# Performance work log

Hardware: AMD Instinct MI355X
Metric: run time of the kernel (lower is better)

Reference implementation:

```python
import jax, jax.numpy as jnp
import numpy as np

NUM_EXPERTS = 8
TOPK = 2
INPUT_DIM = 2048
OUTPUT_DIM = 2048


def setup_inputs() -> dict:
    key = jax.random.key(0)
    k_x, k_w, k_gw, k_gb = jax.random.split(key, 4)
    x = jax.random.normal(k_x, (8192, INPUT_DIM), dtype=jnp.float32)
    # experts: Linear(input_dim, output_dim*num_experts), xavier_uniform weight, zero bias
    fan_out = OUTPUT_DIM * NUM_EXPERTS
    limit = float(np.sqrt(6.0 / (INPUT_DIM + fan_out)))
    expert_w = jax.random.uniform(k_w, (fan_out, INPUT_DIM), minval=-limit, maxval=limit, dtype=jnp.float32)
    expert_b = jnp.zeros((fan_out,), dtype=jnp.float32)
    # gate: Linear(input_dim, num_experts), default torch init (uniform +-1/sqrt(fan_in))
    gl = 1.0 / float(np.sqrt(INPUT_DIM))
    gate_w = jax.random.uniform(k_gw, (NUM_EXPERTS, INPUT_DIM), minval=-gl, maxval=gl, dtype=jnp.float32)
    gate_b = jax.random.uniform(k_gb, (NUM_EXPERTS,), minval=-gl, maxval=gl, dtype=jnp.float32)
    return {"x": x, "expert_w": expert_w, "expert_b": expert_b, "gate_w": gate_w, "gate_b": gate_b}


def reference(x, expert_w, expert_b, gate_w, gate_b):
    B = x.shape[0]
    # gating
    gate_logits = x @ gate_w.T + gate_b                      # [B, E]
    gate_probs = jax.nn.softmax(gate_logits, axis=-1)
    top_k_probs, top_k_idx = jax.lax.top_k(gate_probs, TOPK)  # [B, K]
    # dense expert GEMM: all experts computed
    expert_out = x @ expert_w.T + expert_b                   # [B, E*D_out]
    expert_out = expert_out.reshape(B, NUM_EXPERTS, OUTPUT_DIM)
    # gather selected experts per token and combine
    sel = jnp.take_along_axis(expert_out, top_k_idx[:, :, None], axis=1)  # [B, K, D_out]
    out = jnp.sum(sel * top_k_probs[:, :, None], axis=1)     # [B, D_out]
    return out
```

## Files before the change

kernel.cpp:

```cpp
#include <hip/hip_runtime.h>

#define NUM_TOKENS 8192
#define DIM 2048
#define NE 8
#define BM 128
#define BN 128
#define BK 64

typedef __bf16 bf16x8 __attribute__((ext_vector_type(8)));
typedef float f32x4 __attribute__((ext_vector_type(4)));

typedef __attribute__((address_space(1))) const void* as1_cvp;
typedef __attribute__((address_space(3))) void* as3_vp;

__device__ __forceinline__ unsigned short f2bf(float f) {
  unsigned int u = __float_as_uint(f);
  unsigned int lsb = (u >> 16) & 1u;
  u += 0x7fffu + lsb;
  return (unsigned short)(u >> 16);
}
__device__ __forceinline__ float bflo(unsigned int u) {
  return __uint_as_float(u << 16);
}
__device__ __forceinline__ float bfhi(unsigned int u) {
  return __uint_as_float(u & 0xffff0000u);
}

__global__ __launch_bounds__(256) void convert_w_kernel(
    const float4* __restrict__ w, ushort4* __restrict__ wb) {
  int i = blockIdx.x * 256 + threadIdx.x;
  float4 v = w[i];
  ushort4 o;
  o.x = f2bf(v.x); o.y = f2bf(v.y); o.z = f2bf(v.z); o.w = f2bf(v.w);
  wb[i] = o;
}

__global__ __launch_bounds__(256) void gating_kernel(
    const float* __restrict__ x, const float* __restrict__ gw,
    const float* __restrict__ gb, unsigned short* __restrict__ xb,
    float* __restrict__ probs, int* __restrict__ routed) {
  const int wave = threadIdx.x >> 6;
  const int lane = threadIdx.x & 63;
  const int t = blockIdx.x * 4 + wave;
  const float4* xrow = (const float4*)(x + (size_t)t * DIM);
  ushort4* xbrow = (ushort4*)(xb + (size_t)t * DIM);
  float acc[NE];
#pragma unroll
  for (int e = 0; e < NE; ++e) acc[e] = 0.f;
#pragma unroll
  for (int it = 0; it < DIM / (4 * 64); ++it) {
    const int k4 = it * 64 + lane;
    float4 xv = xrow[k4];
    ushort4 o;
    o.x = f2bf(xv.x); o.y = f2bf(xv.y); o.z = f2bf(xv.z); o.w = f2bf(xv.w);
    xbrow[k4] = o;
#pragma unroll
    for (int e = 0; e < NE; ++e) {
      float4 wv = ((const float4*)(gw + (size_t)e * DIM))[k4];
      acc[e] += xv.x * wv.x + xv.y * wv.y + xv.z * wv.z + xv.w * wv.w;
    }
  }
#pragma unroll
  for (int e = 0; e < NE; ++e) {
#pragma unroll
    for (int off = 32; off > 0; off >>= 1)
      acc[e] += __shfl_xor(acc[e], off, 64);
  }
  if (lane == 0) {
    float p[NE];
    float mx = -1e30f;
#pragma unroll
    for (int e = 0; e < NE; ++e) {
      p[e] = acc[e] + gb[e];
      mx = fmaxf(mx, p[e]);
    }
    float s = 0.f;
#pragma unroll
    for (int e = 0; e < NE; ++e) { p[e] = __expf(p[e] - mx); s += p[e]; }
    float inv = 1.f / s;
#pragma unroll
    for (int e = 0; e < NE; ++e) p[e] *= inv;
    int e0 = 0;
#pragma unroll
    for (int e = 1; e < NE; ++e) if (p[e] > p[e0]) e0 = e;
    int e1 = (e0 == 0) ? 1 : 0;
#pragma unroll
    for (int e = 0; e < NE; ++e) if (e != e0 && p[e] > p[e1]) e1 = e;
    probs[t * 2 + 0] = p[e0];
    probs[t * 2 + 1] = p[e1];
    routed[t] = e0 | (e1 << 8);
  }
}

__global__ __launch_bounds__(256) void build_lists_kernel(
    const int* __restrict__ routed, int* __restrict__ lists,
    int* __restrict__ counts, int* __restrict__ tokpos) {
  const int e = blockIdx.x;
  const int tid = threadIdx.x;
  __shared__ int sc[256];
  __shared__ int sb[256];
  const int base_t = tid * (NUM_TOKENS / 256);
  int c = 0, cb = 0;
#pragma unroll 4
  for (int j = 0; j < NUM_TOKENS / 256; ++j) {
    int r = routed[base_t + j];
    int a0 = r & 0xff, a1 = (r >> 8) & 0xff;
    c += (a0 == e) + (a1 == e);
    cb += (a0 < e) + (a1 < e);
  }
  sc[tid] = c;
  sb[tid] = cb;
  __syncthreads();
  for (int ofs = 1; ofs < 256; ofs <<= 1) {
    int v = (tid >= ofs) ? sc[tid - ofs] : 0;
    int w = (tid >= ofs) ? sb[tid - ofs] : 0;
    __syncthreads();
    sc[tid] += v;
    sb[tid] += w;
    __syncthreads();
  }
  const int ebase = sb[255];
  int pos = sc[tid] - c;
#pragma unroll 4
  for (int j = 0; j < NUM_TOKENS / 256; ++j) {
    int t = base_t + j;
    int r = routed[t];
    if ((r & 0xff) == e) {
      lists[e * NUM_TOKENS + pos] = t;
      tokpos[2 * t] = ebase + pos;
      pos++;
    }
    if (((r >> 8) & 0xff) == e) {
      lists[e * NUM_TOKENS + pos] = t | 0x10000;
      tokpos[2 * t + 1] = ebase + pos;
      pos++;
    }
  }
  if (tid == 255) {
    counts[e] = sc[255];
    counts[8 + e] = ebase;
  }
}

__global__ __launch_bounds__(256) void moe_gemm_kernel(
    const unsigned short* __restrict__ xb,
    const unsigned short* __restrict__ wb,
    const float* __restrict__ eb,
    const float* __restrict__ probs,
    const int* __restrict__ lists,
    const int* __restrict__ counts,
    unsigned short* __restrict__ y,
    float* __restrict__ out,
    int use_y) {
  const int e = blockIdx.z;
  const int cnt = counts[e];
  const int s = blockIdx.x + 16 * blockIdx.y;
  const int xcd = s & 7;
  const int j = s >> 3;
  const int R = (j >> 4) * 8 + xcd;
  const int w4 = j & 15;
  const int mt = (R >> 2) * 4 + (w4 & 3);
  const int nt = (R & 3) * 4 + (w4 >> 2);
  const int m0 = mt * BM;
  if (m0 >= cnt) return;
  const int n0 = nt * BN;

  __shared__ __attribute__((aligned(16))) unsigned short As[BM * BK];
  __shared__ __attribute__((aligned(16))) unsigned short Bs[BN * BK];

  const int tid = threadIdx.x;
  const int wave = tid >> 6;
  const int lane = tid & 63;
  const int srow = lane >> 3;
  const int scol = ((lane & 7) ^ srow) * 8;

  const unsigned short* ag[4];
  const unsigned short* bg[4];
#pragma unroll
  for (int i = 0; i < 4; ++i) {
    int r = m0 + wave * 32 + i * 8 + srow;
    int rc = r < cnt ? r : cnt - 1;
    int tok = lists[e * NUM_TOKENS + rc] & 0xFFFF;
    ag[i] = xb + (size_t)tok * DIM + scol;
    int wr = e * DIM + n0 + wave * 32 + i * 8 + srow;
    bg[i] = wb + (size_t)wr * DIM + scol;
  }

  const f32x4 zero = {0.f, 0.f, 0.f, 0.f};
  f32x4 acc[4][4];
#pragma unroll
  for (int a = 0; a < 4; ++a)
#pragma unroll
    for (int b = 0; b < 4; ++b) acc[a][b] = zero;

  const int wm = (wave >> 1) * 64;
  const int wn = (wave & 1) * 64;
  const int frow = lane & 15;
  const int csel = lane >> 4;
  const int swz = lane & 7;

  for (int k0 = 0; k0 < DIM; k0 += BK) {
    __syncthreads();
#pragma unroll
    for (int i = 0; i < 4; ++i) {
      __builtin_amdgcn_global_load_lds(
          (as1_cvp)(ag[i] + k0),
          (as3_vp)(As + (wave * 32 + i * 8) * BK), 16, 0, 0);
      __builtin_amdgcn_global_load_lds(
          (as1_cvp)(bg[i] + k0),
          (as3_vp)(Bs + (wave * 32 + i * 8) * BK), 16, 0, 0);
    }
    __syncthreads();
#pragma unroll
    for (int kk = 0; kk < BK; kk += 32) {
      const int koff = ((((kk >> 3) | csel) ^ swz) << 3);
      bf16x8 af[4], bfr[4];
#pragma unroll
      for (int im = 0; im < 4; ++im)
        af[im] = *(const bf16x8*)(As + (wm + im * 16 + frow) * BK + koff);
#pragma unroll
      for (int in_ = 0; in_ < 4; ++in_)
        bfr[in_] = *(const bf16x8*)(Bs + (wn + in_ * 16 + frow) * BK + koff);
#pragma unroll
      for (int im = 0; im < 4; ++im)
#pragma unroll
        for (int in_ = 0; in_ < 4; ++in_)
          acc[im][in_] = __builtin_amdgcn_mfma_f32_16x16x32_bf16(
              af[im], bfr[in_], acc[im][in_], 0, 0, 0);
    }
  }

  const int quad = lane >> 4;
  const int col = lane & 15;
  const int ybase = counts[8 + e];
#pragma unroll
  for (int im = 0; im < 4; ++im) {
#pragma unroll
    for (int reg = 0; reg < 4; ++reg) {
      int r = m0 + wm + im * 16 + quad * 4 + reg;
      if (r >= cnt) continue;
      if (use_y) {
        unsigned short* yrow = y + (size_t)(ybase + r) * DIM;
#pragma unroll
        for (int in_ = 0; in_ < 4; ++in_) {
          int n = n0 + wn + in_ * 16 + col;
          yrow[n] = f2bf(acc[im][in_][reg] + eb[e * DIM + n]);
        }
      } else {
        int entry = lists[e * NUM_TOKENS + r];
        int tok = entry & 0xFFFF;
        int slot = entry >> 16;
        float p = probs[tok * 2 + slot];
        float* orow = out + (size_t)tok * DIM;
#pragma unroll
        for (int in_ = 0; in_ < 4; ++in_) {
          int n = n0 + wn + in_ * 16 + col;
          float v = acc[im][in_][reg] + eb[e * DIM + n];
          atomicAdd(orow + n, p * v);
        }
      }
    }
  }
}

__global__ __launch_bounds__(256) void combine_kernel(
    const unsigned short* __restrict__ y, const float* __restrict__ probs,
    const int* __restrict__ tokpos, float* __restrict__ out) {
  const int t = blockIdx.x;
  const int tid = threadIdx.x;
  const int i0 = tokpos[2 * t], i1 = tokpos[2 * t + 1];
  const float p0 = probs[2 * t], p1 = probs[2 * t + 1];
  uint4 a = ((const uint4*)(y + (size_t)i0 * DIM))[tid];
  uint4 b = ((const uint4*)(y + (size_t)i1 * DIM))[tid];
  float4 o0, o1;
  o0.x = p0 * bflo(a.x) + p1 * bflo(b.x);
  o0.y = p0 * bfhi(a.x) + p1 * bfhi(b.x);
  o0.z = p0 * bflo(a.y) + p1 * bflo(b.y);
  o0.w = p0 * bfhi(a.y) + p1 * bfhi(b.y);
  o1.x = p0 * bflo(a.z) + p1 * bflo(b.z);
  o1.y = p0 * bfhi(a.z) + p1 * bfhi(b.z);
  o1.z = p0 * bflo(a.w) + p1 * bflo(b.w);
  o1.w = p0 * bfhi(a.w) + p1 * bfhi(b.w);
  float4* orow = (float4*)(out + (size_t)t * DIM);
  orow[2 * tid] = o0;
  orow[2 * tid + 1] = o1;
}

extern "C" void kernel_launch(void* const* d_in, const int* in_sizes, int n_in,
                              void* d_out, int out_size, void* d_ws, size_t ws_size,
                              hipStream_t stream) {
  const float* x  = (const float*)d_in[0];
  const float* ew = (const float*)d_in[1];
  const float* eb = (const float*)d_in[2];
  const float* gw = (const float*)d_in[3];
  const float* gb = (const float*)d_in[4];
  float* out = (float*)d_out;
  char* p = (char*)d_ws;

  const size_t NEED = 67108864ull + 33554432ull + 67108864ull + 65536ull +
                      262144ull + 64ull + 32768ull + 65536ull;
  const int use_y = (ws_size >= NEED) ? 1 : 0;

  unsigned short* wb = (unsigned short*)p; p += 67108864;
  unsigned short* xb = (unsigned short*)p; p += 33554432;
  unsigned short* y = nullptr;
  if (use_y) { y = (unsigned short*)p; p += 67108864; }
  float* probs = (float*)p; p += 65536;
  int* lists   = (int*)p;   p += 262144;
  int* counts  = (int*)p;   p += 64;
  int* routed  = (int*)p;   p += 32768;
  int* tokpos  = (int*)p;   p += 65536;

  if (!use_y)
    hipMemsetAsync(out, 0, (size_t)NUM_TOKENS * DIM * sizeof(float), stream);
  convert_w_kernel<<<(NE * DIM * DIM / 4) / 256, 256, 0, stream>>>(
      (const float4*)ew, (ushort4*)wb);
  gating_kernel<<<NUM_TOKENS / 4, 256, 0, stream>>>(x, gw, gb, xb, probs,
                                                    routed);
  build_lists_kernel<<<NE, 256, 0, stream>>>(routed, lists, counts, tokpos);
  moe_gemm_kernel<<<dim3(DIM / BN, NUM_TOKENS / BM, NE), 256, 0, stream>>>(
      xb, wb, eb, probs, lists, counts, y, out, use_y);
  if (use_y)
    combine_kernel<<<NUM_TOKENS, 256, 0, stream>>>(y, probs, tokpos, out);
}
```

Baseline: 505.5 us.

## Fuse weight conversion into gating kernel, vectorize GEMM epilogue, widen list builder

Merges the weight bf16 conversion and the gating/x-conversion into one launch, removing a kernel boundary and letting the two memory-bound phases overlap. Swaps the MFMA operands so each lane holds four consecutive output columns, which allows 8-byte vectorized bf16 stores and float4 bias loads in the epilogue in place of scattered 2-byte stores. Doubles the build_lists block to 512 threads to shorten each thread's serial scan. The counts buffer padding is also enlarged slightly.

```diff
diff --git a/kernel.cpp b/kernel.cpp
--- a/kernel.cpp
+++ b/kernel.cpp
@@ -26,19 +26,19 @@
   return __uint_as_float(u & 0xffff0000u);
 }
 
-__global__ __launch_bounds__(256) void convert_w_kernel(
-    const float4* __restrict__ w, ushort4* __restrict__ wb) {
-  int i = blockIdx.x * 256 + threadIdx.x;
-  float4 v = w[i];
-  ushort4 o;
-  o.x = f2bf(v.x); o.y = f2bf(v.y); o.z = f2bf(v.z); o.w = f2bf(v.w);
-  wb[i] = o;
-}
-
-__global__ __launch_bounds__(256) void gating_kernel(
+__global__ __launch_bounds__(256) void prep_kernel(
     const float* __restrict__ x, const float* __restrict__ gw,
-    const float* __restrict__ gb, unsigned short* __restrict__ xb,
+    const float* __restrict__ gb, const float4* __restrict__ w,
+    ushort4* __restrict__ wb, unsigned short* __restrict__ xb,
     float* __restrict__ probs, int* __restrict__ routed) {
+  if (blockIdx.x >= NUM_TOKENS / 4) {
+    int i = (blockIdx.x - NUM_TOKENS / 4) * 256 + threadIdx.x;
+    float4 v = w[i];
+    ushort4 o;
+    o.x = f2bf(v.x); o.y = f2bf(v.y); o.z = f2bf(v.z); o.w = f2bf(v.w);
+    wb[i] = o;
+    return;
+  }
   const int wave = threadIdx.x >> 6;
   const int lane = threadIdx.x & 63;
   const int t = blockIdx.x * 4 + wave;
@@ -92,17 +92,17 @@
   }
 }
 
-__global__ __launch_bounds__(256) void build_lists_kernel(
+__global__ __launch_bounds__(512) void build_lists_kernel(
     const int* __restrict__ routed, int* __restrict__ lists,
     int* __restrict__ counts, int* __restrict__ tokpos) {
   const int e = blockIdx.x;
   const int tid = threadIdx.x;
-  __shared__ int sc[256];
-  __shared__ int sb[256];
-  const int base_t = tid * (NUM_TOKENS / 256);
+  __shared__ int sc[512];
+  __shared__ int sb[512];
+  const int base_t = tid * (NUM_TOKENS / 512);
   int c = 0, cb = 0;
 #pragma unroll 4
-  for (int j = 0; j < NUM_TOKENS / 256; ++j) {
+  for (int j = 0; j < NUM_TOKENS / 512; ++j) {
     int r = routed[base_t + j];
     int a0 = r & 0xff, a1 = (r >> 8) & 0xff;
     c += (a0 == e) + (a1 == e);
@@ -111,7 +111,7 @@
   sc[tid] = c;
   sb[tid] = cb;
   __syncthreads();
-  for (int ofs = 1; ofs < 256; ofs <<= 1) {
+  for (int ofs = 1; ofs < 512; ofs <<= 1) {
     int v = (tid >= ofs) ? sc[tid - ofs] : 0;
     int w = (tid >= ofs) ? sb[tid - ofs] : 0;
     __syncthreads();
@@ -119,10 +119,10 @@
     sb[tid] += w;
     __syncthreads();
   }
-  const int ebase = sb[255];
+  const int ebase = sb[511];
   int pos = sc[tid] - c;
 #pragma unroll 4
-  for (int j = 0; j < NUM_TOKENS / 256; ++j) {
+  for (int j = 0; j < NUM_TOKENS / 512; ++j) {
     int t = base_t + j;
     int r = routed[t];
     if ((r & 0xff) == e) {
@@ -136,8 +136,8 @@
       pos++;
     }
   }
-  if (tid == 255) {
-    counts[e] = sc[255];
+  if (tid == 511) {
+    counts[e] = sc[511];
     counts[8 + e] = ebase;
   }
 }
@@ -226,38 +226,45 @@
 #pragma unroll
         for (int in_ = 0; in_ < 4; ++in_)
           acc[im][in_] = __builtin_amdgcn_mfma_f32_16x16x32_bf16(
-              af[im], bfr[in_], acc[im][in_], 0, 0, 0);
+              bfr[in_], af[im], acc[im][in_], 0, 0, 0);
     }
   }
 
   const int quad = lane >> 4;
-  const int col = lane & 15;
   const int ybase = counts[8 + e];
 #pragma unroll
   for (int im = 0; im < 4; ++im) {
-#pragma unroll
-    for (int reg = 0; reg < 4; ++reg) {
-      int r = m0 + wm + im * 16 + quad * 4 + reg;
-      if (r >= cnt) continue;
-      if (use_y) {
-        unsigned short* yrow = y + (size_t)(ybase + r) * DIM;
-#pragma unroll
-        for (int in_ = 0; in_ < 4; ++in_) {
-          int n = n0 + wn + in_ * 16 + col;
-          yrow[n] = f2bf(acc[im][in_][reg] + eb[e * DIM + n]);
-        }
-      } else {
-        int entry = lists[e * NUM_TOKENS + r];
-        int tok = entry & 0xFFFF;
-        int slot = entry >> 16;
-        float p = probs[tok * 2 + slot];
-        float* orow = out + (size_t)tok * DIM;
-#pragma unroll
-        for (int in_ = 0; in_ < 4; ++in_) {
-          int n = n0 + wn + in_ * 16 + col;
-          float v = acc[im][in_][reg] + eb[e * DIM + n];
-          atomicAdd(orow + n, p * v);
-        }
+    int r = m0 + wm + im * 16 + frow;
+    if (r >= cnt) continue;
+    if (use_y) {
+      unsigned short* yrow = y + (size_t)(ybase + r) * DIM;
+#pragma unroll
+      for (int in_ = 0; in_ < 4; ++in_) {
+        int n = n0 + wn + in_ * 16 + quad * 4;
+        float4 ebv = *(const float4*)(eb + (size_t)e * DIM + n);
+        f32x4 v = acc[im][in_];
+        ushort4 o;
+        o.x = f2bf(v[0] + ebv.x);
+        o.y = f2bf(v[1] + ebv.y);
+        o.z = f2bf(v[2] + ebv.z);
+        o.w = f2bf(v[3] + ebv.w);
+        *(ushort4*)(yrow + n) = o;
+      }
+    } else {
+      int entry = lists[e * NUM_TOKENS + r];
+      int tok = entry & 0xFFFF;
+      int slot = entry >> 16;
+      float pw = probs[tok * 2 + slot];
+      float* orow = out + (size_t)tok * DIM;
+#pragma unroll
+      for (int in_ = 0; in_ < 4; ++in_) {
+        int n = n0 + wn + in_ * 16 + quad * 4;
+        float4 ebv = *(const float4*)(eb + (size_t)e * DIM + n);
+        f32x4 v = acc[im][in_];
+        atomicAdd(orow + n + 0, pw * (v[0] + ebv.x));
+        atomicAdd(orow + n + 1, pw * (v[1] + ebv.y));
+        atomicAdd(orow + n + 2, pw * (v[2] + ebv.z));
+        atomicAdd(orow + n + 3, pw * (v[3] + ebv.w));
       }
     }
   }
@@ -298,7 +305,7 @@
   char* p = (char*)d_ws;
 
   const size_t NEED = 67108864ull + 33554432ull + 67108864ull + 65536ull +
-                      262144ull + 64ull + 32768ull + 65536ull;
+                      262144ull + 128ull + 32768ull + 65536ull;
   const int use_y = (ws_size >= NEED) ? 1 : 0;
 
   unsigned short* wb = (unsigned short*)p; p += 67108864;
@@ -307,17 +314,15 @@
   if (use_y) { y = (unsigned short*)p; p += 67108864; }
   float* probs = (float*)p; p += 65536;
   int* lists   = (int*)p;   p += 262144;
-  int* counts  = (int*)p;   p += 64;
+  int* counts  = (int*)p;   p += 128;
   int* routed  = (int*)p;   p += 32768;
   int* tokpos  = (int*)p;   p += 65536;
 
   if (!use_y)
     hipMemsetAsync(out, 0, (size_t)NUM_TOKENS * DIM * sizeof(float), stream);
-  convert_w_kernel<<<(NE * DIM * DIM / 4) / 256, 256, 0, stream>>>(
-      (const float4*)ew, (ushort4*)wb);
-  gating_kernel<<<NUM_TOKENS / 4, 256, 0, stream>>>(x, gw, gb, xb, probs,
-                                                    routed);
-  build_lists_kernel<<<NE, 256, 0, stream>>>(routed, lists, counts, tokpos);
+  prep_kernel<<<NUM_TOKENS / 4 + (NE * DIM * DIM / 4) / 256, 256, 0, stream>>>(
+      x, gw, gb, (const float4*)ew, (ushort4*)wb, xb, probs, routed);
+  build_lists_kernel<<<NE, 512, 0, stream>>>(routed, lists, counts, tokpos);
   moe_gemm_kernel<<<dim3(DIM / BN, NUM_TOKENS / BM, NE), 256, 0, stream>>>(
       xb, wb, eb, probs, lists, counts, y, out, use_y);
   if (use_y)
```

New measurement: 503.1 us. No clear change (-0.5%).
